# Kernel optimization log

Measured on AMD Instinct MI355X. Metric: run time of the kernel, lower is better.

Reference implementation:

```python
import jax, jax.numpy as jnp
import numpy as np

DIM = 1024
INTER = 512
E = 32            # n_routed_experts
TOPK = 4          # n_activated_experts
GROUPS = 8        # n_expert_groups
TOPK_GROUPS = 4
SHARED_INTER = 2 * INTER  # n_shared_experts * moe_inter_dim
ROUTE_SCALE = 1.0
B, S = 8, 4096


def setup_inputs() -> dict:
    key = jax.random.key(0)
    ks = jax.random.split(key, 16)
    def xav(k, shape):
        fan_in, fan_out = shape[-2], shape[-1]
        lim = np.sqrt(6.0 / (fan_in + fan_out))
        return jax.random.uniform(k, shape, jnp.float32, -lim, lim)
    return {
        "x": jax.random.normal(ks[0], (B, S, DIM), jnp.float32),
        "gw": xav(ks[1], (DIM, E)),
        "gb": jnp.zeros((E,), jnp.float32),
        "w1": xav(ks[2], (E, DIM, INTER)),
        "b1": jnp.zeros((E, INTER), jnp.float32),
        "w3": xav(ks[3], (E, DIM, INTER)),
        "b3": jnp.zeros((E, INTER), jnp.float32),
        "w2": xav(ks[4], (E, INTER, DIM)),
        "b2": jnp.zeros((E, DIM), jnp.float32),
        "sw1": xav(ks[5], (DIM, SHARED_INTER)),
        "sb1": jnp.zeros((SHARED_INTER,), jnp.float32),
        "sw3": xav(ks[6], (DIM, SHARED_INTER)),
        "sb3": jnp.zeros((SHARED_INTER,), jnp.float32),
        "sw2": xav(ks[7], (SHARED_INTER, DIM)),
        "sb2": jnp.zeros((DIM,), jnp.float32),
    }


def _gate(xf, gw, gb):
    # scores: softmax over routed experts in fp32 (score_func='softmax')
    T = xf.shape[0]
    scores = jax.nn.softmax((xf @ gw + gb).astype(jnp.float32), axis=-1)  # [T, E]
    original_scores = scores
    # group-masked routing (n_expert_groups > 1)
    scores_g = scores.reshape(T, GROUPS, E // GROUPS)                     # [T, G, E/G]
    group_scores = jnp.sum(jax.lax.top_k(scores_g, 2)[0], axis=-1)        # [T, G]
    gidx = jax.lax.top_k(group_scores, TOPK_GROUPS)[1]                    # [T, topk_groups]
    keep = jnp.zeros((T, GROUPS), bool).at[jnp.arange(T)[:, None], gidx].set(True)
    masked = jnp.where(keep[:, :, None], scores_g, -jnp.inf).reshape(T, E)
    indices = jax.lax.top_k(masked, TOPK)[1]                              # [T, topk]
    weights = jnp.take_along_axis(original_scores, indices, axis=1) * ROUTE_SCALE
    return weights.astype(xf.dtype), indices


def reference(x, gw, gb, w1, b1, w3, b3, w2, b2, sw1, sb1, sw3, sb3, sw2, sb2):
    shape = x.shape
    xf = x.reshape(-1, DIM)                                               # [T, dim]
    T = xf.shape[0]
    weights, indices = _gate(xf, gw, gb)
    # dense combine weights [T, E]: w_e(t) = routing weight if expert e chosen for t else 0
    cw = jnp.zeros((T, E), xf.dtype).at[jnp.arange(T)[:, None], indices].add(weights)
    # scan over experts: y += w_e * SwiGLU_e(x). Zero weight -> zero contribution,
    # identical math to the masked dispatch/scatter-add in the torch code.
    def body(y, p):
        w1e, b1e, w3e, b3e, w2e, b2e, we = p
        h = jax.nn.silu(xf @ w1e + b1e) * (xf @ w3e + b3e)                # [T, inter]
        return y + we[:, None] * (h @ w2e + b2e), None
    y0 = jnp.zeros_like(xf)
    y, _ = jax.lax.scan(body, y0, (w1, b1, w3, b3, w2, b2, cw.T))
    # shared experts MLP (SwiGLU)
    z = (jax.nn.silu(xf @ sw1 + sb1) * (xf @ sw3 + sb3)) @ sw2 + sb2
    return (y + z).reshape(shape)
```

## Files before the change

### kernel.cpp

```cpp
#include <hip/hip_runtime.h>
#include <stdint.h>

#define DIM_    1024
#define INTER_  512

typedef short bf16x4 __attribute__((ext_vector_type(4)));
typedef short bf16x8 __attribute__((ext_vector_type(8)));
typedef float f32x4  __attribute__((ext_vector_type(4)));

__device__ __forceinline__ unsigned short f2bf(float f) {
  union { float f; unsigned u; } v; v.f = f;
  return (unsigned short)((v.u + 0x7FFFu + ((v.u >> 16) & 1u)) >> 16);
}
__device__ __forceinline__ unsigned f2bf2(float a, float b) {
  union { float f; unsigned u; } va, vb; va.f = a; vb.f = b;
  unsigned ra = (va.u + 0x7FFFu + ((va.u >> 16) & 1u)) >> 16;
  unsigned rb = (vb.u + 0x7FFFu + ((vb.u >> 16) & 1u)) >> 16;
  return ra | (rb << 16);
}
__device__ __forceinline__ float bfhi(unsigned u) {
  union { unsigned u; float f; } v; v.u = u & 0xffff0000u; return v.f;
}
__device__ __forceinline__ float bflo(unsigned u) {
  union { unsigned u; float f; } v; v.u = u << 16; return v.f;
}

__device__ __forceinline__ void gl16(const void* g, void* l) {
  __builtin_amdgcn_global_load_lds(
      (const __attribute__((address_space(1))) unsigned int*)g,
      (__attribute__((address_space(3))) unsigned int*)l, 16, 0, 0);
}

#define BARX() do { asm volatile("" ::: "memory"); \
                    __builtin_amdgcn_s_barrier();  \
                    asm volatile("" ::: "memory"); } while (0)

__global__ __launch_bounds__(256) void gate_kernel(
    const float* __restrict__ x, const float* __restrict__ gw,
    const float* __restrict__ gb, int* __restrict__ idx, float* __restrict__ wts,
    unsigned short* __restrict__ xb) {
  __shared__ double s_sc[4][32];
  __shared__ double s_gs[4][8];
  const int wid = threadIdx.x >> 6, lane = threadIdx.x & 63;
  const int t = blockIdx.x * 4 + wid;
  {
    const float* xrow = x + (size_t)t * DIM_ + lane * 16;
    unsigned short* xbrow = xb + (size_t)t * DIM_ + lane * 16;
    float4 f0 = *(const float4*)(xrow);
    float4 f1 = *(const float4*)(xrow + 4);
    float4 f2v = *(const float4*)(xrow + 8);
    float4 f3v = *(const float4*)(xrow + 12);
    uint4 o0, o1;
    o0.x = f2bf2(f0.x, f0.y);  o0.y = f2bf2(f0.z, f0.w);
    o0.z = f2bf2(f1.x, f1.y);  o0.w = f2bf2(f1.z, f1.w);
    o1.x = f2bf2(f2v.x, f2v.y); o1.y = f2bf2(f2v.z, f2v.w);
    o1.z = f2bf2(f3v.x, f3v.y); o1.w = f2bf2(f3v.z, f3v.w);
    *(uint4*)(xbrow) = o0;
    *(uint4*)(xbrow + 8) = o1;
  }
  const int e = lane & 31, half = lane >> 5;
  const float* xr  = x  + (size_t)t * DIM_ + half * 512;
  const float* gwp = gw + (size_t)half * 512 * 32 + e;
  double a0 = 0, a1 = 0, a2 = 0, a3 = 0;
  for (int k = 0; k < 512; k += 4) {
    float4 xv = *(const float4*)(xr + k);
    a0 += (double)xv.x * (double)gwp[(k + 0) * 32];
    a1 += (double)xv.y * (double)gwp[(k + 1) * 32];
    a2 += (double)xv.z * (double)gwp[(k + 2) * 32];
    a3 += (double)xv.w * (double)gwp[(k + 3) * 32];
  }
  double lg = (a0 + a1) + (a2 + a3);
  lg += __shfl_xor(lg, 32);
  lg += (double)gb[e];
  double m = lg;
  #pragma unroll
  for (int d = 1; d < 32; d <<= 1) m = fmax(m, __shfl_xor(m, d));
  double ex = exp(lg - m);
  double ssum = ex;
  #pragma unroll
  for (int d = 1; d < 32; d <<= 1) ssum += __shfl_xor(ssum, d);
  double sc = ex / ssum;
  double p  = __shfl_xor(sc, 1);
  double m1 = fmax(sc, p), n1 = fmin(sc, p);
  double m2 = __shfl_xor(m1, 2), n2 = __shfl_xor(n1, 2);
  double gs = (m1 >= m2) ? (m1 + fmax(n1, m2)) : (m2 + fmax(n2, m1));
  if (lane < 32) {
    s_sc[wid][e] = sc;
    if ((e & 3) == 0) s_gs[wid][e >> 2] = gs;
  }
  __syncthreads();
  if (lane == 0) {
    unsigned kmask = 0;
    for (int it = 0; it < 4; ++it) {
      int bg = 0; double bv = -1.0;
      for (int g = 0; g < 8; ++g)
        if (!((kmask >> g) & 1u) && s_gs[wid][g] > bv) { bv = s_gs[wid][g]; bg = g; }
      kmask |= 1u << bg;
    }
    unsigned umask = 0;
    for (int slot = 0; slot < 4; ++slot) {
      int be = 0; double bv = -1.0;
      for (int ee = 0; ee < 32; ++ee)
        if (((kmask >> (ee >> 2)) & 1u) && !((umask >> ee) & 1u) && s_sc[wid][ee] > bv) {
          bv = s_sc[wid][ee]; be = ee;
        }
      umask |= 1u << be;
      idx[t * 4 + slot] = be;
      wts[t * 4 + slot] = (float)bv;
    }
  }
}

__global__ __launch_bounds__(256) void count_kernel(const int* __restrict__ idx,
                                                    int* __restrict__ meta) {
  __shared__ int h[32];
  int tid = threadIdx.x;
  if (tid < 32) h[tid] = 0;
  __syncthreads();
  atomicAdd(&h[idx[blockIdx.x * 256 + tid]], 1);
  __syncthreads();
  if (tid < 32 && h[tid]) atomicAdd(&meta[tid], h[tid]);
}

__global__ void scan_kernel(int* __restrict__ meta) {
  int lane = threadIdx.x & 63;
  if (lane < 32) {
    int c = meta[lane];
    int pre = c;
    #pragma unroll
    for (int d = 1; d < 32; d <<= 1) { int t = __shfl_up(pre, d); if (lane >= d) pre += t; }
    int excl = pre - c;
    meta[64 + lane] = excl;
    meta[32 + lane] = excl;
    int nt = (c + 255) >> 8;
    int ntp = nt;
    #pragma unroll
    for (int d = 1; d < 32; d <<= 1) { int t = __shfl_up(ntp, d); if (lane >= d) ntp += t; }
    int ntExcl = ntp - nt;
    for (int k = 0; k < nt; ++k) { meta[128 + ntExcl + k] = lane; meta[1184 + ntExcl + k] = k << 8; }
    if (lane == 31) { meta[96] = excl + c; meta[97] = ntExcl + nt; }
  }
}

__global__ __launch_bounds__(256) void scatter_kernel(
    const int* __restrict__ idx, int* __restrict__ meta,
    int* __restrict__ tok, int* __restrict__ inv) {
  int i = blockIdx.x * 256 + threadIdx.x;
  int lane = threadIdx.x & 63;
  int e = idx[i];
  unsigned long long m = ~0ull;
  #pragma unroll
  for (int b = 0; b < 5; ++b) {
    unsigned long long vote = __ballot((e >> b) & 1);
    m &= ((e >> b) & 1) ? vote : ~vote;
  }
  int leader = __ffsll((long long)m) - 1;
  int rank = __popcll(m & ((1ull << lane) - 1));
  int base = 0;
  if (lane == leader) base = atomicAdd(&meta[32 + e], (int)__popcll(m));
  base = __shfl(base, leader);
  int p = base + rank;
  tok[p] = i >> 2;
  inv[i] = p;
}

__global__ __launch_bounds__(256) void repack_kernel(
    const float* __restrict__ src, unsigned short* __restrict__ dst,
    int K, int N, int tilesPerMat) {
  const int w = blockIdx.x * 4 + (threadIdx.x >> 6);
  const int j = threadIdx.x & 63;
  const int e = w / tilesPerMat, rem = w % tilesPerMat;
  const int kSteps = K >> 5;
  const int nt = rem / kSteps, kq = rem % kSteps;
  const float* s = src + (size_t)e * K * N + (size_t)(kq * 32) * N + nt * 64 + j;
  float v[32];
  #pragma unroll
  for (int kk = 0; kk < 32; ++kk) v[kk] = s[(size_t)kk * N];
  char* d = (char*)dst + (size_t)w * 4096 + j * 64;
  const int sz = (j & 3) ^ ((j >> 2) & 3);
  #pragma unroll
  for (int q = 0; q < 4; ++q) {
    int o = (q ^ sz) * 8;
    uint4 tv;
    tv.x = f2bf2(v[o + 0], v[o + 1]);
    tv.y = f2bf2(v[o + 2], v[o + 3]);
    tv.z = f2bf2(v[o + 4], v[o + 5]);
    tv.w = f2bf2(v[o + 6], v[o + 7]);
    *(uint4*)(d + q * 16) = tv;
  }
}

__global__ __launch_bounds__(256) void repack13_kernel(
    const float* __restrict__ src1, const float* __restrict__ src3,
    unsigned short* __restrict__ dst, int K, int N, int jtTiles) {
  const int w = blockIdx.x * 4 + (threadIdx.x >> 6);
  const int j = threadIdx.x & 63;
  const int kSteps = K >> 5;
  const int tpm = jtTiles * kSteps;
  const int e = w / tpm, rem = w % tpm;
  const int jt = rem / kSteps, kq = rem % kSteps;
  const int jg = jt * 64 + j;
  const int c = ((jg >> 5) << 4) + (jg & 15);
  const float* s = (((jg >> 4) & 1) ? src3 : src1)
                 + (size_t)e * K * N + (size_t)(kq * 32) * N + c;
  float v[32];
  #pragma unroll
  for (int kk = 0; kk < 32; ++kk) v[kk] = s[(size_t)kk * N];
  char* d = (char*)dst + (size_t)w * 4096 + j * 64;
  const int sz = (j & 3) ^ ((j >> 2) & 3);
  #pragma unroll
  for (int q = 0; q < 4; ++q) {
    int o = (q ^ sz) * 8;
    uint4 tv;
    tv.x = f2bf2(v[o + 0], v[o + 1]);
    tv.y = f2bf2(v[o + 2], v[o + 3]);
    tv.z = f2bf2(v[o + 4], v[o + 5]);
    tv.w = f2bf2(v[o + 6], v[o + 7]);
    *(uint4*)(d + q * 16) = tv;
  }
}


#define G8_PRE()                                                              \
  const int tid = threadIdx.x, lane = tid & 63, wave = tid >> 6;              \
  const int wm = wave >> 2, wn = wave & 3;                                    \
  const int f = lane & 15, g = lane >> 4;                                     \
  const int wud = wave >> 2, wlo = wave & 3;                                  \
  const int row_in = wlo * 16 + (lane >> 2);                                  \
  const int szr = (row_in & 3) ^ ((row_in >> 2) & 3);                         \
  const int qs = (((lane & 3) ^ szr) << 4);                                   \
  const int btile_off = wlo * 1024 + lane * 16;                               \
  const int wv1k = wave * 1024;                                               \
  const int awb = wm * 8192;                                                  \
  const int wn4 = wn * 4096;                                                  \
  int aoff[4];                                                                \
  _Pragma("unroll")                                                           \
  for (int ii = 0; ii < 4; ++ii) {                                            \
    int u16 = ii * 16 + f;                                                    \
    aoff[ii] = u16 * 64 + ((g ^ ((u16 & 3) ^ ((u16 >> 2) & 3))) << 4);        \
  }                                                                           \
  bf16x8 bvp[4];                                                              \
  f32x4 acc[8][4];                                                            \
  const f32x4 zz = {0.f, 0.f, 0.f, 0.f};                                      \
  _Pragma("unroll")                                                           \
  for (int mi = 0; mi < 8; ++mi)                                              \
    _Pragma("unroll")                                                         \
    for (int ni = 0; ni < 4; ++ni) acc[mi][ni] = zz;

#define G8_PH(p, UMAXv)                                                       \
  {                                                                           \
    const char* sb_ = lds + ((p) >> 1) * 32768;                               \
    const char* ab_ = sb_ + awb + ((p) & 1) * 4096;                           \
    bf16x8 af_[4];                                                            \
    _Pragma("unroll")                                                         \
    for (int mi = 0; mi < 4; ++mi) af_[mi] = *(const bf16x8*)(ab_ + aoff[mi]);\
    if (!((p) & 1)) {                                                         \
      const char* bb_ = sb_ + 16384 + wn4;                                    \
      _Pragma("unroll")                                                       \
      for (int ni = 0; ni < 4; ++ni)                                          \
        bvp[ni] = *(const bf16x8*)(bb_ + aoff[ni]);                           \
    }                                                                         \
    int u_ = I4 + 3 + ((p) >> 1);                                             \
    if (u_ >= (UMAXv)) u_ = (UMAXv) - 1;                                      \
    char* td_ = lds + (((((p) >> 1) + 3) & 3) * 32768);                       \
    if ((p) & 1) {                                                            \
      gl16(pB0 + (size_t)u_ * 4096, td_ + 16384 + wv1k);                      \
      gl16(pB1 + (size_t)u_ * 4096, td_ + 24576 + wv1k);                      \
    } else {                                                                  \
      gl16(pA0 + u_ * 64, td_ + wv1k);                                        \
      gl16(pA1 + u_ * 64, td_ + 8192 + wv1k);                                 \
    }                                                                         \
    BARX();                                                                   \
    __builtin_amdgcn_s_setprio(1);                                            \
    _Pragma("unroll")                                                         \
    for (int ni = 0; ni < 4; ++ni)                                            \
      _Pragma("unroll")                                                       \
      for (int mi = 0; mi < 4; ++mi)                                          \
        acc[((p) & 1) * 4 + mi][ni] = __builtin_amdgcn_mfma_f32_16x16x32_bf16(\
            af_[mi], bvp[ni], acc[((p) & 1) * 4 + mi][ni], 0, 0, 0);          \
    __builtin_amdgcn_s_setprio(0);                                            \
    if ((p) & 1) asm volatile("s_waitcnt vmcnt(8)" ::: "memory");             \
    BARX();                                                                   \
  }

#define G8_BODY(UMAXv)                                                        \
  _Pragma("unroll")                                                           \
  for (int uu = 0; uu < 3; ++uu) {                                            \
    gl16(pA0 + uu * 64, lds + uu * 32768 + wv1k);                             \
    gl16(pA1 + uu * 64, lds + uu * 32768 + 8192 + wv1k);                      \
    gl16(pB0 + (size_t)uu * 4096, lds + uu * 32768 + 16384 + wv1k);           \
    gl16(pB1 + (size_t)uu * 4096, lds + uu * 32768 + 24576 + wv1k);           \
  }                                                                           \
  asm volatile("s_waitcnt vmcnt(8)" ::: "memory");                            \
  BARX();                                                                     \
  for (int I = 0; I < (UMAXv) / 4; ++I) {                                     \
    const int I4 = I * 4;                                                     \
    G8_PH(0, UMAXv); G8_PH(1, UMAXv); G8_PH(2, UMAXv); G8_PH(3, UMAXv);       \
    G8_PH(4, UMAXv); G8_PH(5, UMAXv); G8_PH(6, UMAXv); G8_PH(7, UMAXv);       \
  }

#define XCD_SWZ(GXv)                                                          \
  const int nb_ = gridDim.x;                                                  \
  const int b_ = blockIdx.x;                                                  \
  const int w_ = (b_ & 7) * (nb_ >> 3) + (b_ >> 3);                           \
  const int bx = w_ % (GXv);                                                  \
  const int by = w_ / (GXv);

__global__ __launch_bounds__(512, 2) void s1_kernel(
    const unsigned short* __restrict__ xb, const unsigned short* __restrict__ w13,
    const float* __restrict__ sb1, const float* __restrict__ sb3,
    unsigned short* __restrict__ Hs) {
  __shared__ char lds[131072];
  XCD_SWZ(8);
  const int m0 = by * 256;
  G8_PRE();
  const char* pA0 = (const char*)xb + (size_t)(m0 + wud * 64 + row_in) * 2048 + qs;
  const char* pA1 = pA0 + (size_t)128 * 2048;
  const char* pB0 = (const char*)w13 + ((size_t)(bx * 4 + wud) * 32) * 4096 + btile_off;
  const char* pB1 = (const char*)w13 + ((size_t)(bx * 4 + 2 + wud) * 32) * 4096 + btile_off;
  G8_BODY(32);
  const int colb = bx * 128;
  #pragma unroll
  for (int p2 = 0; p2 < 2; ++p2) {
    int c = colb + wn * 32 + p2 * 16 + f;
    float bb1 = sb1[c], bb3 = sb3[c];
    #pragma unroll
    for (int m8 = 0; m8 < 8; ++m8) {
      int row = m0 + wm * 128 + (m8 >> 2) * 64 + (m8 & 3) * 16 + g * 4;
      #pragma unroll
      for (int r = 0; r < 4; ++r) {
        float v1 = acc[m8][2 * p2][r] + bb1;
        float v3 = acc[m8][2 * p2 + 1][r] + bb3;
        float h = (v1 / (1.f + __expf(-v1))) * v3;
        Hs[(size_t)(row + r) * 1024 + c] = f2bf(h);
      }
    }
  }
}

__global__ __launch_bounds__(512, 2) void s2_kernel(
    const unsigned short* __restrict__ Hs, const unsigned short* __restrict__ b2i,
    const float* __restrict__ sb2, float* __restrict__ out) {
  __shared__ char lds[131072];
  XCD_SWZ(4);
  const int m0 = by * 256;
  G8_PRE();
  const char* pA0 = (const char*)Hs + (size_t)(m0 + wud * 64 + row_in) * 2048 + qs;
  const char* pA1 = pA0 + (size_t)128 * 2048;
  const char* pB0 = (const char*)b2i + ((size_t)(bx * 4 + wud) * 32) * 4096 + btile_off;
  const char* pB1 = (const char*)b2i + ((size_t)(bx * 4 + 2 + wud) * 32) * 4096 + btile_off;
  G8_BODY(32);
  #pragma unroll
  for (int ni = 0; ni < 4; ++ni) {
    int c = bx * 256 + wn * 64 + ni * 16 + f;
    float bb = sb2[c];
    #pragma unroll
    for (int m8 = 0; m8 < 8; ++m8) {
      int row = m0 + wm * 128 + (m8 >> 2) * 64 + (m8 & 3) * 16 + g * 4;
      #pragma unroll
      for (int r = 0; r < 4; ++r)
        out[(size_t)(row + r) * 1024 + c] = acc[m8][ni][r] + bb;
    }
  }
}

__global__ __launch_bounds__(512, 2) void g1_kernel(
    const unsigned short* __restrict__ xb, const unsigned short* __restrict__ w13,
    const float* __restrict__ b1, const float* __restrict__ b3,
    const int* __restrict__ tok, const int* __restrict__ meta,
    unsigned short* __restrict__ H) {
  __shared__ char lds[131072];
  XCD_SWZ(4);
  if (by >= meta[97]) return;
  const int e = meta[128 + by], m0 = meta[1184 + by];
  const int off_e = meta[64 + e], nrem = meta[e] - m0;
  G8_PRE();
  const int r0a = wud * 64 + row_in;
  const int ix0 = off_e + m0 + ((r0a < nrem) ? r0a : 0);
  const int ix1 = off_e + m0 + ((r0a + 128 < nrem) ? r0a + 128 : 0);
  const char* pA0 = (const char*)xb + (size_t)tok[ix0] * 2048 + qs;
  const char* pA1 = (const char*)xb + (size_t)tok[ix1] * 2048 + qs;
  const char* pB0 = (const char*)w13 + ((size_t)(e * 16 + bx * 4 + wud) * 32) * 4096 + btile_off;
  const char* pB1 = (const char*)w13 + ((size_t)(e * 16 + bx * 4 + 2 + wud) * 32) * 4096 + btile_off;
  G8_BODY(32);
  const int colb = bx * 128;
  #pragma unroll
  for (int p2 = 0; p2 < 2; ++p2) {
    int c = colb + wn * 32 + p2 * 16 + f;
    float bb1 = b1[e * 512 + c], bb3 = b3[e * 512 + c];
    #pragma unroll
    for (int m8 = 0; m8 < 8; ++m8) {
      int row = wm * 128 + (m8 >> 2) * 64 + (m8 & 3) * 16 + g * 4;
      #pragma unroll
      for (int r = 0; r < 4; ++r) {
        if (row + r < nrem) {
          float v1 = acc[m8][2 * p2][r] + bb1;
          float v3 = acc[m8][2 * p2 + 1][r] + bb3;
          float h = (v1 / (1.f + __expf(-v1))) * v3;
          H[(size_t)(off_e + m0 + row + r) * 512 + c] = f2bf(h);
        }
      }
    }
  }
}

__global__ __launch_bounds__(512, 2) void g2_kernel(
    const unsigned short* __restrict__ H, const unsigned short* __restrict__ w2i,
    const float* __restrict__ b2, const int* __restrict__ meta,
    unsigned short* __restrict__ Y, int cbase) {
  __shared__ char lds[131072];
  XCD_SWZ(2);
  if (by >= meta[97]) return;
  const int e = meta[128 + by], m0 = meta[1184 + by];
  const int off_e = meta[64 + e], nrem = meta[e] - m0;
  G8_PRE();
  const int r0a = wud * 64 + row_in;
  const int ix0 = off_e + m0 + ((r0a < nrem) ? r0a : 0);
  const int ix1 = off_e + m0 + ((r0a + 128 < nrem) ? r0a + 128 : 0);
  const char* pA0 = (const char*)H + (size_t)ix0 * 1024 + qs;
  const char* pA1 = (const char*)H + (size_t)ix1 * 1024 + qs;
  const int nt0 = (cbase >> 6) + bx * 4;
  const char* pB0 = (const char*)w2i + ((size_t)(e * 16 + nt0 + wud) * 16) * 4096 + btile_off;
  const char* pB1 = (const char*)w2i + ((size_t)(e * 16 + nt0 + 2 + wud) * 16) * 4096 + btile_off;
  G8_BODY(16);
  #pragma unroll
  for (int ni = 0; ni < 4; ++ni) {
    int ycol = bx * 256 + wn * 64 + ni * 16 + f;
    float bb = b2[e * 1024 + cbase + ycol];
    #pragma unroll
    for (int m8 = 0; m8 < 8; ++m8) {
      int row = wm * 128 + (m8 >> 2) * 64 + (m8 & 3) * 16 + g * 4;
      #pragma unroll
      for (int r = 0; r < 4; ++r) {
        if (row + r < nrem)
          Y[(size_t)(off_e + m0 + row + r) * 512 + ycol] = f2bf(acc[m8][ni][r] + bb);
      }
    }
  }
}

__global__ __launch_bounds__(256) void combine_kernel(
    const unsigned short* __restrict__ Y, const int* __restrict__ inv,
    const float* __restrict__ wts, float* __restrict__ out, int cbase) {
  int t = blockIdx.x * 2 + (threadIdx.x >> 7);
  int c = (threadIdx.x & 127) * 4;
  int4 iv = *(const int4*)(inv + t * 4);
  float4 wv = *(const float4*)(wts + t * 4);
  float* op = out + (size_t)t * 1024 + cbase + c;
  float4 o = *(float4*)op;
  uint2 u;
  u = *(const uint2*)(Y + (size_t)iv.x * 512 + c);
  o.x += wv.x * bflo(u.x); o.y += wv.x * bfhi(u.x);
  o.z += wv.x * bflo(u.y); o.w += wv.x * bfhi(u.y);
  u = *(const uint2*)(Y + (size_t)iv.y * 512 + c);
  o.x += wv.y * bflo(u.x); o.y += wv.y * bfhi(u.x);
  o.z += wv.y * bflo(u.y); o.w += wv.y * bfhi(u.y);
  u = *(const uint2*)(Y + (size_t)iv.z * 512 + c);
  o.x += wv.z * bflo(u.x); o.y += wv.z * bfhi(u.x);
  o.z += wv.z * bflo(u.y); o.w += wv.z * bfhi(u.y);
  u = *(const uint2*)(Y + (size_t)iv.w * 512 + c);
  o.x += wv.w * bflo(u.x); o.y += wv.w * bfhi(u.x);
  o.z += wv.w * bflo(u.y); o.w += wv.w * bfhi(u.y);
  *(float4*)op = o;
}

extern "C" void kernel_launch(void* const* d_in, const int* in_sizes, int n_in,
                              void* d_out, int out_size, void* d_ws, size_t ws_size,
                              hipStream_t stream) {
  const float* x   = (const float*)d_in[0];
  const float* gw  = (const float*)d_in[1];
  const float* gb  = (const float*)d_in[2];
  const float* w1  = (const float*)d_in[3];
  const float* b1  = (const float*)d_in[4];
  const float* w3  = (const float*)d_in[5];
  const float* b3  = (const float*)d_in[6];
  const float* w2  = (const float*)d_in[7];
  const float* b2  = (const float*)d_in[8];
  const float* sw1 = (const float*)d_in[9];
  const float* sb1 = (const float*)d_in[10];
  const float* sw3 = (const float*)d_in[11];
  const float* sb3 = (const float*)d_in[12];
  const float* sw2 = (const float*)d_in[13];
  const float* sb2 = (const float*)d_in[14];
  float* out = (float*)d_out;
  char* ws = (char*)d_ws;

  const size_t OFF_XB   = 134217728;
  const size_t OFF_W13I = 201326592;
  const size_t OFF_W2I  = 268435456;
  const size_t OFF_S13I = 301989888;
  const size_t OFF_SW2I = 306184192;
  const size_t OFF_IDX  = 308281344;
  const size_t OFF_WTS  = 308805632;
  const size_t OFF_TOK  = 309329920;
  const size_t OFF_INV  = 309854208;
  const size_t OFF_META = 310378496;
  if (ws_size < OFF_META + 8960) return;

  unsigned short* H    = (unsigned short*)ws;
  unsigned short* xb   = (unsigned short*)(ws + OFF_XB);
  unsigned short* Yb   = (unsigned short*)(ws + OFF_XB);
  unsigned short* w13i = (unsigned short*)(ws + OFF_W13I);
  unsigned short* w2i  = (unsigned short*)(ws + OFF_W2I);
  unsigned short* s13i = (unsigned short*)(ws + OFF_S13I);
  unsigned short* sw2i = (unsigned short*)(ws + OFF_SW2I);
  int*   idx  = (int*)(ws + OFF_IDX);
  float* wts  = (float*)(ws + OFF_WTS);
  int*   tokl = (int*)(ws + OFF_TOK);
  int*   inv  = (int*)(ws + OFF_INV);
  int*   meta = (int*)(ws + OFF_META);

  hipMemsetAsync(meta, 0, 128, stream);
  gate_kernel<<<dim3(8192), dim3(256), 0, stream>>>(x, gw, gb, idx, wts, xb);
  count_kernel<<<dim3(512), dim3(256), 0, stream>>>(idx, meta);
  scan_kernel<<<dim3(1), dim3(64), 0, stream>>>(meta);
  scatter_kernel<<<dim3(512), dim3(256), 0, stream>>>(idx, meta, tokl, inv);
  repack13_kernel<<<dim3(4096), dim3(256), 0, stream>>>(w1, w3, w13i, 1024, 512, 16);
  repack_kernel<<<dim3(2048), dim3(256), 0, stream>>>(w2, w2i, 512, 1024, 256);
  repack13_kernel<<<dim3(256), dim3(256), 0, stream>>>(sw1, sw3, s13i, 1024, 1024, 32);
  repack_kernel<<<dim3(128), dim3(256), 0, stream>>>(sw2, sw2i, 1024, 1024, 512);
  s1_kernel<<<dim3(1024), dim3(512), 0, stream>>>(xb, s13i, sb1, sb3, H);
  s2_kernel<<<dim3(512), dim3(512), 0, stream>>>(H, sw2i, sb2, out);
  g1_kernel<<<dim3(2176), dim3(512), 0, stream>>>(xb, w13i, b1, b3, tokl, meta, H);
  g2_kernel<<<dim3(1088), dim3(512), 0, stream>>>(H, w2i, b2, meta, Yb, 0);
  combine_kernel<<<dim3(16384), dim3(256), 0, stream>>>(Yb, inv, wts, out, 0);
  g2_kernel<<<dim3(1088), dim3(512), 0, stream>>>(H, w2i, b2, meta, Yb, 512);
  combine_kernel<<<dim3(16384), dim3(256), 0, stream>>>(Yb, inv, wts, out, 512);
}
```

Before: 1.592 ms.

## Double-buffer LDS fragment registers so reads overlap MFMA in GEMM main loop

Restructures the GEMM inner-loop phases so the A/B fragments for the next phase are read from LDS into a second register set while MFMAs run on the current set (ping-pong af0/af1, bv0/bv1). Each stage's global-to-LDS prefetch is now issued in one phase instead of split across two, and the waitcnt/barrier placement changes to one barrier per phase. The aim is to hide LDS read latency behind matrix instructions. In exchange it raises register pressure, which at 512 threads with 2 blocks per CU could cause spills.

```diff
diff --git a/kernel.cpp b/kernel.cpp
--- a/kernel.cpp
+++ b/kernel.cpp
@@ -239,7 +239,6 @@
     int u16 = ii * 16 + f;                                                    \
     aoff[ii] = u16 * 64 + ((g ^ ((u16 & 3) ^ ((u16 >> 2) & 3))) << 4);        \
   }                                                                           \
-  bf16x8 bvp[4];                                                              \
   f32x4 acc[8][4];                                                            \
   const f32x4 zz = {0.f, 0.f, 0.f, 0.f};                                      \
   _Pragma("unroll")                                                           \
@@ -247,40 +246,48 @@
     _Pragma("unroll")                                                         \
     for (int ni = 0; ni < 4; ++ni) acc[mi][ni] = zz;
 
-#define G8_PH(p, UMAXv)                                                       \
+#define G8_EVEN(s, AFC, AFN, BVC, UMAXv)                                      \
   {                                                                           \
-    const char* sb_ = lds + ((p) >> 1) * 32768;                               \
-    const char* ab_ = sb_ + awb + ((p) & 1) * 4096;                           \
-    bf16x8 af_[4];                                                            \
+    BARX();                                                                   \
+    int u_ = I4 + 3 + (s); if (u_ >= (UMAXv)) u_ = (UMAXv) - 1;               \
+    char* td_ = lds + ((((s) + 3) & 3) * 32768);                              \
+    gl16(pA0 + u_ * 64, td_ + wv1k);                                          \
+    gl16(pA1 + u_ * 64, td_ + 8192 + wv1k);                                   \
+    gl16(pB0 + (size_t)u_ * 4096, td_ + 16384 + wv1k);                        \
+    gl16(pB1 + (size_t)u_ * 4096, td_ + 24576 + wv1k);                        \
+    const char* cb_ = lds + (((s) & 3) * 32768);                              \
     _Pragma("unroll")                                                         \
-    for (int mi = 0; mi < 4; ++mi) af_[mi] = *(const bf16x8*)(ab_ + aoff[mi]);\
-    if (!((p) & 1)) {                                                         \
-      const char* bb_ = sb_ + 16384 + wn4;                                    \
-      _Pragma("unroll")                                                       \
-      for (int ni = 0; ni < 4; ++ni)                                          \
-        bvp[ni] = *(const bf16x8*)(bb_ + aoff[ni]);                           \
-    }                                                                         \
-    int u_ = I4 + 3 + ((p) >> 1);                                             \
-    if (u_ >= (UMAXv)) u_ = (UMAXv) - 1;                                      \
-    char* td_ = lds + (((((p) >> 1) + 3) & 3) * 32768);                       \
-    if ((p) & 1) {                                                            \
-      gl16(pB0 + (size_t)u_ * 4096, td_ + 16384 + wv1k);                      \
-      gl16(pB1 + (size_t)u_ * 4096, td_ + 24576 + wv1k);                      \
-    } else {                                                                  \
-      gl16(pA0 + u_ * 64, td_ + wv1k);                                        \
-      gl16(pA1 + u_ * 64, td_ + 8192 + wv1k);                                 \
-    }                                                                         \
-    BARX();                                                                   \
+    for (int mi = 0; mi < 4; ++mi)                                            \
+      AFN[mi] = *(const bf16x8*)(cb_ + awb + 4096 + aoff[mi]);                \
     __builtin_amdgcn_s_setprio(1);                                            \
     _Pragma("unroll")                                                         \
     for (int ni = 0; ni < 4; ++ni)                                            \
       _Pragma("unroll")                                                       \
       for (int mi = 0; mi < 4; ++mi)                                          \
-        acc[((p) & 1) * 4 + mi][ni] = __builtin_amdgcn_mfma_f32_16x16x32_bf16(\
-            af_[mi], bvp[ni], acc[((p) & 1) * 4 + mi][ni], 0, 0, 0);          \
+        acc[mi][ni] = __builtin_amdgcn_mfma_f32_16x16x32_bf16(                \
+            AFC[mi], BVC[ni], acc[mi][ni], 0, 0, 0);                          \
     __builtin_amdgcn_s_setprio(0);                                            \
-    if ((p) & 1) asm volatile("s_waitcnt vmcnt(8)" ::: "memory");             \
+    asm volatile("s_waitcnt vmcnt(4)" ::: "memory");                          \
+  }
+
+#define G8_ODD(s, AFC, BVC, AFN, BVN)                                         \
+  {                                                                           \
     BARX();                                                                   \
+    const char* nb_ = lds + ((((s) + 1) & 3) * 32768);                        \
+    _Pragma("unroll")                                                         \
+    for (int mi = 0; mi < 4; ++mi)                                            \
+      AFN[mi] = *(const bf16x8*)(nb_ + awb + aoff[mi]);                       \
+    _Pragma("unroll")                                                         \
+    for (int ni = 0; ni < 4; ++ni)                                            \
+      BVN[ni] = *(const bf16x8*)(nb_ + 16384 + wn4 + aoff[ni]);               \
+    __builtin_amdgcn_s_setprio(1);                                            \
+    _Pragma("unroll")                                                         \
+    for (int ni = 0; ni < 4; ++ni)                                            \
+      _Pragma("unroll")                                                       \
+      for (int mi = 0; mi < 4; ++mi)                                          \
+        acc[4 + mi][ni] = __builtin_amdgcn_mfma_f32_16x16x32_bf16(            \
+            AFC[mi], BVC[ni], acc[4 + mi][ni], 0, 0, 0);                      \
+    __builtin_amdgcn_s_setprio(0);                                            \
   }
 
 #define G8_BODY(UMAXv)                                                        \
@@ -293,10 +300,19 @@
   }                                                                           \
   asm volatile("s_waitcnt vmcnt(8)" ::: "memory");                            \
   BARX();                                                                     \
+  bf16x8 af0[4], af1[4], bv0[4], bv1[4];                                      \
+  _Pragma("unroll")                                                           \
+  for (int mi = 0; mi < 4; ++mi)                                              \
+    af0[mi] = *(const bf16x8*)(lds + awb + aoff[mi]);                         \
+  _Pragma("unroll")                                                           \
+  for (int ni = 0; ni < 4; ++ni)                                              \
+    bv0[ni] = *(const bf16x8*)(lds + 16384 + wn4 + aoff[ni]);                 \
   for (int I = 0; I < (UMAXv) / 4; ++I) {                                     \
     const int I4 = I * 4;                                                     \
-    G8_PH(0, UMAXv); G8_PH(1, UMAXv); G8_PH(2, UMAXv); G8_PH(3, UMAXv);       \
-    G8_PH(4, UMAXv); G8_PH(5, UMAXv); G8_PH(6, UMAXv); G8_PH(7, UMAXv);       \
+    G8_EVEN(0, af0, af1, bv0, UMAXv); G8_ODD(0, af1, bv0, af0, bv1);          \
+    G8_EVEN(1, af0, af1, bv1, UMAXv); G8_ODD(1, af1, bv1, af0, bv0);          \
+    G8_EVEN(2, af0, af1, bv0, UMAXv); G8_ODD(2, af1, bv0, af0, bv1);          \
+    G8_EVEN(3, af0, af1, bv1, UMAXv); G8_ODD(3, af1, bv1, af0, bv0);          \
   }
 
 #define XCD_SWZ(GXv)                                                          \
```

Result: no change. 1.566 ms (-1.7%).
